# Kernel optimization log

Hardware: AMD Instinct MI355X
Metric: run time of the kernel (lower is better)

Reference implementation:

```python
import jax, jax.numpy as jnp
import numpy as np

H = 8
HID = 512
DH = HID // H
EPS = 1e-5


def _ln(x, g, b):
    mu = jnp.mean(x, axis=-1, keepdims=True)
    var = jnp.mean(jnp.square(x - mu), axis=-1, keepdims=True)
    return (x - mu) * jax.lax.rsqrt(var + EPS) * g + b


def setup_inputs() -> dict:
    key = jax.random.key(0)
    ks = jax.random.split(key, 40)
    L, M, P, D = 4096, 1024, 4096, 512

    def xav(k, shp):
        lim = np.sqrt(6.0 / (shp[0] + shp[1]))
        return jax.random.uniform(k, shp, jnp.float32, -lim, lim)

    inp = {
        'lncRNA_embedding': jax.random.normal(ks[0], (L, D), jnp.float32),
        'miRNA_embedding': jax.random.normal(ks[1], (M, D), jnp.float32),
        'protein_embedding': jax.random.normal(ks[2], (P, D), jnp.float32),
        'lncRNA_miRNA_matrix': jax.random.randint(ks[3], (L, M), 0, 2, jnp.int32),
        'protein_miRNA_matrix': jax.random.randint(ks[4], (P, M), 0, 2, jnp.int32),
    }
    names = ['Wl', 'Wm', 'Wp', 'Wql', 'Wkl', 'Wvl', 'Wqp', 'Wkp', 'Wvp']
    for i, n in enumerate(names):
        inp[n] = xav(ks[5 + i], (HID, HID))
        inp['b' + n[1:]] = jnp.zeros((HID,), jnp.float32)
    inp['Wml'] = xav(ks[20], (2 * HID, D // 2))
    inp['bml'] = jnp.zeros((D // 2,), jnp.float32)
    inp['Wmp'] = xav(ks[21], (2 * HID, D // 2))
    inp['bmp'] = jnp.zeros((D // 2,), jnp.float32)
    inp['g1'] = jnp.ones((D // 2,), jnp.float32)
    inp['be1'] = jnp.zeros((D // 2,), jnp.float32)
    inp['g2'] = jnp.ones((D // 2,), jnp.float32)
    inp['be2'] = jnp.zeros((D // 2,), jnp.float32)
    # first three linears take dim-D input (D == HID here)
    return inp


def reference(lncRNA_embedding, miRNA_embedding, protein_embedding,
              lncRNA_miRNA_matrix, protein_miRNA_matrix,
              Wl, bl, Wm, bm, Wp, bp,
              Wql, bql, Wkl, bkl, Wvl, bvl,
              Wqp, bqp, Wkp, bkp, Wvp, bvp,
              Wml, bml, Wmp, bmp, g1, be1, g2, be2):
    L = lncRNA_embedding.shape[0]
    M = miRNA_embedding.shape[0]
    P = protein_embedding.shape[0]

    lt = lncRNA_embedding @ Wl + bl          # [L, HID]
    mt = miRNA_embedding @ Wm + bm           # [M, HID]
    pt = protein_embedding @ Wp + bp         # [P, HID]

    def heads(x, W, b, n):
        return (x @ W + b).reshape(n, H, DH)

    Ql = heads(lt, Wql, bql, L)              # [L, H, DH]
    Kl = heads(mt, Wkl, bkl, M)
    Vl = heads(mt, Wvl, bvl, M)
    Qp = heads(pt, Wqp, bqp, P)
    Kp = heads(mt, Wkp, bkp, M)
    Vp = heads(mt, Wvp, bvp, M)

    scale = 1.0 / np.sqrt(DH)
    sl = jnp.einsum('lhd,mhd->hlm', Ql, Kl) * scale      # [H, L, M]
    sl = jnp.where(lncRNA_miRNA_matrix[None] == 0, -1e9, sl)
    awl = jax.nn.softmax(sl, axis=-1)

    sp = jnp.einsum('phd,mhd->hpm', Qp, Kp) * scale      # [H, P, M]
    sp = jnp.where(protein_miRNA_matrix[None] == 0, -1e9, sp)
    awp = jax.nn.softmax(sp, axis=-1)

    ctx_l = jax.nn.relu(jnp.einsum('hlm,mhd->lhd', awl, Vl).reshape(L, HID))
    ctx_p = jax.nn.relu(jnp.einsum('hpm,mhd->phd', awp, Vp).reshape(P, HID))

    mutual = jnp.einsum('hlm,hpm->lp', awl, awp) / H     # [L, P]

    fin_l = ctx_l + mutual @ ctx_p
    fin_p = ctx_p + mutual.T @ ctx_l

    out_l = _ln(jnp.concatenate([lt, fin_l], axis=-1) @ Wml + bml, g1, be1)
    out_p = _ln(jnp.concatenate([fin_p, pt], axis=-1) @ Wmp + bmp, g2, be2)
    return out_l, out_p
```

## Files before the change

### kernel.cpp

```cpp
#include <hip/hip_runtime.h>
#include <hip/hip_bf16.h>

using bf16 = __hip_bfloat16;
typedef __attribute__((ext_vector_type(8))) short short8;
typedef __attribute__((ext_vector_type(4))) float floatx4;
typedef __attribute__((ext_vector_type(8))) unsigned short ushort8;
typedef __attribute__((ext_vector_type(4))) int i32x4;
typedef __attribute__((ext_vector_type(8))) int i32x8;

__device__ __forceinline__ float b2f(unsigned short u) {
    union { unsigned int i; float f; } x; x.i = ((unsigned int)u) << 16; return x.f;
}

__device__ __forceinline__ void async16(const void* g, void* l) {
    __builtin_amdgcn_global_load_lds((const __attribute__((address_space(1))) void*)g,
                                     (__attribute__((address_space(3))) void*)l,
                                     16, 0, 0);
}

__device__ __forceinline__ unsigned char f2e4m3(float f) {
    unsigned s = (__float_as_uint(f) >> 24) & 0x80u;
    f = fminf(fabsf(f), 448.f);
    if (f < 0.015625f) {
        int d = (int)rintf(f * 512.f);
        return (unsigned char)(s | (unsigned)d);
    }
    int E = (int)((__float_as_uint(f) >> 23) & 255u) - 127;
    float ulp_inv = __uint_as_float((unsigned)(127 + 3 - E) << 23);
    int m = (int)rintf(f * ulp_inv);
    int n = (m == 16) ? ((E + 8) << 3) : (((E + 7) << 3) + (m - 8));
    if (n > 0x7E) n = 0x7E;
    return (unsigned char)(s | (unsigned)n);
}

__device__ __forceinline__ bool sniff_wave(const unsigned short* p) {
    const int lane = threadIdx.x & 63;
    int wild = 0;
#pragma unroll
    for (int j = 0; j < 4; ++j) {
        float a = fabsf(b2f(p[lane * 4 + j]));
        wild += !(a <= 1e4f);
    }
#pragma unroll
    for (int o = 1; o < 64; o <<= 1) wild += __shfl_xor(wild, o);
    return wild > 16;
}

struct Cvt { const void* src; bf16* dst; int n; };
struct PrepArgs {
    Cvt cv[18];
    const void* tsrc[11];
    bf16* tdst[11];
    const unsigned short* sn;
};

__global__ __launch_bounds__(256) void prep(PrepArgs a) {
    const bool f32 = sniff_wave(a.sn);
    const int y = blockIdx.y;
    __shared__ bf16 tile[32][33];

    if (y < 18) {
        const Cvt c = a.cv[y];
        const int stride = gridDim.x * 256 * 8;
        for (int i = (blockIdx.x * 256 + threadIdx.x) * 8; i < c.n; i += stride) {
            if (f32) {
                const float* s = (const float*)c.src + i;
#pragma unroll
                for (int j = 0; j < 8; ++j) c.dst[i + j] = __float2bfloat16(s[j]);
            } else {
                *(ushort8*)((unsigned short*)c.dst + i) =
                    *(const ushort8*)((const unsigned short*)c.src + i);
            }
        }
        return;
    }

    const int tx = threadIdx.x & 31;
    const int ty = threadIdx.x >> 5;
    if (y < 27) {
        const void* in = a.tsrc[y - 18];
        bf16* out = a.tdst[y - 18];
        const int bc = (blockIdx.x & 15) * 32;
        const int br = (blockIdx.x >> 4) * 32;
#pragma unroll
        for (int i = 0; i < 32; i += 8) {
            const size_t idx = (size_t)(br + ty + i) * 512 + bc + tx;
            tile[ty + i][tx] = f32 ? __float2bfloat16(((const float*)in)[idx])
                                   : ((const bf16*)in)[idx];
        }
        __syncthreads();
#pragma unroll
        for (int i = 0; i < 32; i += 8)
            out[(size_t)(bc + ty + i) * 512 + br + tx] = tile[tx][ty + i];
    } else {
        const void* in = a.tsrc[y - 27 + 9];
        bf16* out = a.tdst[y - 27 + 9];
        const int bc = (blockIdx.x & 7) * 32;
        const int br = (blockIdx.x >> 3) * 32;
#pragma unroll
        for (int i = 0; i < 32; i += 8) {
            const size_t idx = (size_t)(br + ty + i) * 256 + bc + tx;
            tile[ty + i][tx] = f32 ? __float2bfloat16(((const float*)in)[idx])
                                   : ((const bf16*)in)[idx];
        }
        __syncthreads();
#pragma unroll
        for (int i = 0; i < 32; i += 8)
            out[(size_t)(bc + ty + i) * 1024 + br + tx] = tile[tx][ty + i];
    }
}

struct SegTab { const bf16* W[3]; const bf16* bias[3]; bf16* C[3]; int ldc[3]; int rs[3]; };

__global__ __launch_bounds__(256) void gemm_bt_seg(
    const bf16* __restrict__ A, SegTab T, int K)
{
    constexpr int TM = 2, TN = 2;
    __align__(16) __shared__ bf16 As[64 * 64];
    __align__(16) __shared__ bf16 Bs[64 * 64];

    const int lane = threadIdx.x & 63;
    const int wv   = threadIdx.x >> 6;
    const int gm   = blockIdx.y * 64;
    const int seg  = (gm >= 5120) ? 2 : ((gm >= 4096) ? 1 : 0);
    const bf16* B  = T.W[seg];
    const bf16* bias = T.bias[seg];
    bf16* C        = T.C[seg];
    const int ldc  = T.ldc[seg];
    const int m_base = gm - T.rs[seg];
    const int n_base = blockIdx.x * 64;
    const int wm0 = (wv >> 1) * 32;
    const int wn0 = (wv & 1) * 32;

    floatx4 zero = {0.f, 0.f, 0.f, 0.f};
    floatx4 acc[TM][TN];
#pragma unroll
    for (int mt = 0; mt < TM; ++mt)
#pragma unroll
        for (int nt = 0; nt < TN; ++nt) acc[mt][nt] = zero;

    const int sr  = lane >> 3;
    const int sce = ((lane & 7) ^ sr) * 8;
    const int fr  = lane & 15;
    const int q   = lane >> 4;
    const int sw  = fr & 7;

    for (int k0 = 0; k0 < K; k0 += 64) {
#pragma unroll
        for (int cc = 0; cc < 2; ++cc) {
            const int r0t = (wv + cc * 4) * 8;
            async16(A + (size_t)(gm + r0t + sr) * 512 + k0 + sce, &As[r0t * 64]);
            async16(B + (size_t)(n_base + r0t + sr) * 512 + k0 + sce, &Bs[r0t * 64]);
        }
        __syncthreads();
#pragma unroll
        for (int s = 0; s < 2; ++s) {
            const int off = ((s * 4 + q) ^ sw) * 8;
            short8 af[TM], bfr[TN];
#pragma unroll
            for (int mt = 0; mt < TM; ++mt)
                af[mt] = *(const short8*)&As[(wm0 + mt * 16 + fr) * 64 + off];
#pragma unroll
            for (int nt = 0; nt < TN; ++nt)
                bfr[nt] = *(const short8*)&Bs[(wn0 + nt * 16 + fr) * 64 + off];
#pragma unroll
            for (int mt = 0; mt < TM; ++mt)
#pragma unroll
                for (int nt = 0; nt < TN; ++nt)
                    acc[mt][nt] = __builtin_amdgcn_mfma_f32_16x16x32_bf16(
                        af[mt], bfr[nt], acc[mt][nt], 0, 0, 0);
        }
        __syncthreads();
    }

    const int er = lane >> 4;
    const int ec = lane & 15;
#pragma unroll
    for (int nt = 0; nt < TN; ++nt) {
        const int col = n_base + wn0 + nt * 16 + ec;
        const float bv = __bfloat162float(bias[col]);
#pragma unroll
        for (int mt = 0; mt < TM; ++mt)
#pragma unroll
            for (int r = 0; r < 4; ++r) {
                const int row = m_base + wm0 + mt * 16 + er * 4 + r;
                C[(size_t)row * ldc + col] = __float2bfloat16(acc[mt][nt][r] + bv);
            }
    }
}

struct BtArgs { const bf16* A; const bf16* B; void* C; const bf16* bias;
                int lda, ldb, ldc; };
struct BtSet { BtArgs s[3]; };

template <bool F32OUT, bool REMAP2>
__global__ __launch_bounds__(256) void gemm_btx(BtSet P, int K, float scale)
{
    constexpr int TM = 2, TN = 2;
    __align__(16) __shared__ bf16 As[64 * 64];
    __align__(16) __shared__ bf16 Bs[64 * 64];

    const BtArgs g = P.s[blockIdx.z];
    int bx = blockIdx.x, by = blockIdx.y;
    if (REMAP2 && blockIdx.z == 2) {
        const int flat = by * gridDim.x + bx;
        bx = flat & 31; by = flat >> 5;
    }
    const int lane = threadIdx.x & 63;
    const int wv   = threadIdx.x >> 6;
    const int m_base = by * 64;
    const int n_base = bx * 64;
    const int wm0 = (wv >> 1) * 32;
    const int wn0 = (wv & 1) * 32;

    floatx4 zero = {0.f, 0.f, 0.f, 0.f};
    floatx4 acc[TM][TN];
#pragma unroll
    for (int mt = 0; mt < TM; ++mt)
#pragma unroll
        for (int nt = 0; nt < TN; ++nt) acc[mt][nt] = zero;

    const int sr  = lane >> 3;
    const int sce = ((lane & 7) ^ sr) * 8;
    const int fr  = lane & 15;
    const int q   = lane >> 4;
    const int sw  = fr & 7;

    for (int k0 = 0; k0 < K; k0 += 64) {
#pragma unroll
        for (int cc = 0; cc < 2; ++cc) {
            const int r0t = (wv + cc * 4) * 8;
            async16(g.A + (size_t)(m_base + r0t + sr) * g.lda + k0 + sce, &As[r0t * 64]);
            async16(g.B + (size_t)(n_base + r0t + sr) * g.ldb + k0 + sce, &Bs[r0t * 64]);
        }
        __syncthreads();
#pragma unroll
        for (int s = 0; s < 2; ++s) {
            const int off = ((s * 4 + q) ^ sw) * 8;
            short8 af[TM], bfr[TN];
#pragma unroll
            for (int mt = 0; mt < TM; ++mt)
                af[mt] = *(const short8*)&As[(wm0 + mt * 16 + fr) * 64 + off];
#pragma unroll
            for (int nt = 0; nt < TN; ++nt)
                bfr[nt] = *(const short8*)&Bs[(wn0 + nt * 16 + fr) * 64 + off];
#pragma unroll
            for (int mt = 0; mt < TM; ++mt)
#pragma unroll
                for (int nt = 0; nt < TN; ++nt)
                    acc[mt][nt] = __builtin_amdgcn_mfma_f32_16x16x32_bf16(
                        af[mt], bfr[nt], acc[mt][nt], 0, 0, 0);
        }
        __syncthreads();
    }

    const int er = lane >> 4;
    const int ec = lane & 15;
#pragma unroll
    for (int nt = 0; nt < TN; ++nt) {
        const int col = n_base + wn0 + nt * 16 + ec;
        const float bv = __bfloat162float(g.bias[col]);
#pragma unroll
        for (int mt = 0; mt < TM; ++mt)
#pragma unroll
            for (int r = 0; r < 4; ++r) {
                const int row = m_base + wm0 + mt * 16 + er * 4 + r;
                const float v = acc[mt][nt][r] * scale + bv;
                if constexpr (F32OUT)
                    ((float*)g.C)[(size_t)row * g.ldc + col] = v;
                else
                    ((bf16*)g.C)[(size_t)row * g.ldc + col] = __float2bfloat16(v);
            }
    }
}

struct ScArgs { const bf16* Q; const bf16* K; const int* mask; unsigned char* aw;
                unsigned char* awt; };
struct ScSet { ScArgs s[2]; const bf16* vsrc[2]; unsigned char* vdst[2]; };

__global__ __launch_bounds__(256) void scores_v8(ScSet P, int ldk, float scale)
{
    __shared__ float wred[16][4];
    __shared__ float wsum[16][4];
    __shared__ float tile[32][33];

    const int flat = blockIdx.x;
    if (flat >= 4096) {
        const int f2   = flat - 4096;
        const int side = f2 >> 9;
        const int rem  = f2 & 511;
        const bf16* in = P.vsrc[side];
        unsigned char* out = P.vdst[side];
        const int bc = (rem & 15) * 32;
        const int br = (rem >> 4) * 32;
        const int tx = threadIdx.x & 31;
        const int ty = threadIdx.x >> 5;
#pragma unroll
        for (int i = 0; i < 32; i += 8)
            tile[ty + i][tx] =
                __bfloat162float(in[(size_t)(br + ty + i) * 2048 + bc + tx]) * 4.0f;
        __syncthreads();
#pragma unroll
        for (int i = 0; i < 32; i += 8)
            out[(size_t)(bc + ty + i) * 1024 + br + tx] = f2e4m3(tile[tx][ty + i]);
        return;
    }

    const int s    = (flat >> 3) & 3;
    const int unit = (flat >> 5) * 8 + (flat & 7);
    const int side = unit >> 9;
    const int h    = (unit >> 6) & 7;
    const int r0   = (unit & 63) * 64 + s * 16;

    const ScArgs g = P.s[side];
    const int t    = threadIdx.x;
    const int lane = t & 63;
    const int w    = t >> 6;
    const int fr   = lane & 15;
    const int fq   = lane >> 4;
    const int cbase = w * 256;

    const short* Qs = (const short*)g.Q + (size_t)(r0 + fr) * 512 + h * 64 + fq * 8;
    short8 a0 = *(const short8*)(Qs);
    short8 a1 = *(const short8*)(Qs + 32);

    floatx4 accs[16];
    const short* Kb = (const short*)g.K + h * 64 + fq * 8;
#pragma unroll
    for (int c = 0; c < 16; ++c) {
        const int krow = cbase + c * 16 + fr;
        short8 b0 = *(const short8*)(Kb + (size_t)krow * ldk);
        short8 b1 = *(const short8*)(Kb + (size_t)krow * ldk + 32);
        floatx4 acc = {0.f, 0.f, 0.f, 0.f};
        acc = __builtin_amdgcn_mfma_f32_16x16x32_bf16(a0, b0, acc, 0, 0, 0);
        acc = __builtin_amdgcn_mfma_f32_16x16x32_bf16(a1, b1, acc, 0, 0, 0);
        accs[c] = acc;
    }

    float mxr[4] = {-3e38f, -3e38f, -3e38f, -3e38f};
#pragma unroll
    for (int c = 0; c < 16; ++c) {
        const int col = cbase + c * 16 + fr;
#pragma unroll
        for (int r = 0; r < 4; ++r) {
            const int row = r0 + fq * 4 + r;
            float v = (g.mask[(size_t)row * 1024 + col] == 0) ? -1e9f
                                                              : accs[c][r] * scale;
            accs[c][r] = v;
            mxr[r] = fmaxf(mxr[r], v);
        }
    }
#pragma unroll
    for (int o = 1; o < 16; o <<= 1)
#pragma unroll
        for (int r = 0; r < 4; ++r) mxr[r] = fmaxf(mxr[r], __shfl_xor(mxr[r], o));
    if (fr == 0)
#pragma unroll
        for (int r = 0; r < 4; ++r) wred[fq * 4 + r][w] = mxr[r];
    __syncthreads();

    float mx[4], sm[4] = {0.f, 0.f, 0.f, 0.f};
#pragma unroll
    for (int r = 0; r < 4; ++r) {
        const int row = fq * 4 + r;
        mx[r] = fmaxf(fmaxf(wred[row][0], wred[row][1]),
                      fmaxf(wred[row][2], wred[row][3]));
    }
#pragma unroll
    for (int c = 0; c < 16; ++c)
#pragma unroll
        for (int r = 0; r < 4; ++r) {
            float e = __expf(accs[c][r] - mx[r]);
            accs[c][r] = e;
            sm[r] += e;
        }
#pragma unroll
    for (int o = 1; o < 16; o <<= 1)
#pragma unroll
        for (int r = 0; r < 4; ++r) sm[r] += __shfl_xor(sm[r], o);
    if (fr == 0)
#pragma unroll
        for (int r = 0; r < 4; ++r) wsum[fq * 4 + r][w] = sm[r];
    __syncthreads();

    float inv[4];
#pragma unroll
    for (int r = 0; r < 4; ++r) {
        const int row = fq * 4 + r;
        inv[r] = 32.0f / (wsum[row][0] + wsum[row][1] + wsum[row][2] + wsum[row][3]);
    }
#pragma unroll
    for (int c = 0; c < 16; ++c) {
        const int col = cbase + c * 16 + fr;
        unsigned int pk = 0;
#pragma unroll
        for (int r = 0; r < 4; ++r) {
            const int row = r0 + fq * 4 + r;
            const unsigned char qv = f2e4m3(accs[c][r] * inv[r]);
            g.aw[(size_t)row * 8192 + h * 1024 + col] = qv;
            pk |= (unsigned)qv << (8 * r);
        }
        *(unsigned int*)(g.awt + (size_t)(h * 1024 + col) * 4096 + r0 + fq * 4) = pk;
    }
}

struct B8Args { const unsigned char* A; const unsigned char* B; bf16* C;
                unsigned char* CT; };
struct B8Pair { B8Args s[2]; };

__global__ __launch_bounds__(256) void gemm_bt8_ctx(
    B8Pair P, int lda, long long a_kshift, int ldb, int ldc, int ldct,
    int K, float scale)
{
    constexpr int TM = 2, TN = 2;
    __align__(16) __shared__ unsigned char As[64 * 64];
    __align__(16) __shared__ unsigned char Bs[64 * 64];

    const B8Args g = P.s[blockIdx.z];
    const int lane = threadIdx.x & 63;
    const int wv   = threadIdx.x >> 6;
    const int m_base = blockIdx.y * 64;
    const int n_base = blockIdx.x * 64;
    const unsigned char* A = g.A + (long long)blockIdx.x * a_kshift;

    const int wm0 = (wv >> 1) * 32;
    const int wn0 = (wv & 1) * 32;

    floatx4 zero = {0.f, 0.f, 0.f, 0.f};
    floatx4 acc[TM][TN];
#pragma unroll
    for (int mt = 0; mt < TM; ++mt)
#pragma unroll
        for (int nt = 0; nt < TN; ++nt) acc[mt][nt] = zero;

    const int ar = lane >> 2;
    const int ac = (((lane & 3) ^ (ar & 3)) * 16);
    const int fr = lane & 15;
    const int q  = lane >> 4;
    const int sw = fr & 3;

    for (int k0 = 0; k0 < K; k0 += 64) {
        async16(A + (size_t)(m_base + wv * 16 + ar) * lda + k0 + ac, &As[wv * 16 * 64]);
        async16(g.B + (size_t)(n_base + wv * 16 + ar) * ldb + k0 + ac, &Bs[wv * 16 * 64]);
        __syncthreads();
#pragma unroll
        for (int s = 0; s < 2; ++s) {
            const int boff = (((s * 2 + (q >> 1)) ^ sw) * 16) + (q & 1) * 8;
            long af[TM], bfr[TN];
#pragma unroll
            for (int mt = 0; mt < TM; ++mt)
                af[mt] = *(const long*)&As[(wm0 + mt * 16 + fr) * 64 + boff];
#pragma unroll
            for (int nt = 0; nt < TN; ++nt)
                bfr[nt] = *(const long*)&Bs[(wn0 + nt * 16 + fr) * 64 + boff];
#pragma unroll
            for (int mt = 0; mt < TM; ++mt)
#pragma unroll
                for (int nt = 0; nt < TN; ++nt)
                    acc[mt][nt] = __builtin_amdgcn_mfma_f32_16x16x32_fp8_fp8(
                        af[mt], bfr[nt], acc[mt][nt], 0, 0, 0);
        }
        __syncthreads();
    }

    const int er = lane >> 4;
    const int ec = lane & 15;
#pragma unroll
    for (int nt = 0; nt < TN; ++nt) {
        const int col = n_base + wn0 + nt * 16 + ec;
#pragma unroll
        for (int mt = 0; mt < TM; ++mt) {
            const int rowb = m_base + wm0 + mt * 16 + er * 4;
            unsigned int pk = 0;
#pragma unroll
            for (int r = 0; r < 4; ++r) {
                float v = fmaxf(acc[mt][nt][r] * scale, 0.f);
                g.C[(size_t)(rowb + r) * ldc + col] = __float2bfloat16(v);
                pk |= (unsigned)f2e4m3(v * 16.0f) << (8 * r);
            }
            *(unsigned int*)(g.CT + (size_t)col * ldct + rowb) = pk;
        }
    }
}

struct MxArgs { const unsigned char* A; const unsigned char* B; void* C;
                const bf16* Cz; unsigned char* CT; };
struct MxPair { MxArgs s[2]; };

template <int BM, int BN, bool ADDC0, bool FP8OUT, bool TOUT>
__global__ __launch_bounds__(256, 2) void gemm_bt8mx(
    MxPair P, int lda, int ldb, int ldc, int ldc0, int ldct, int K, float scale)
{
    constexpr int WM = BM / 2;
    constexpr int WN = BN / 2;
    constexpr int TM = WM / 16;
    constexpr int TN = WN / 16;

    __align__(16) __shared__ unsigned char As[BM * 128];
    __align__(16) __shared__ unsigned char Bs[BN * 128];

    const MxArgs g = P.s[blockIdx.z];
    const int lane = threadIdx.x & 63;
    const int wv   = threadIdx.x >> 6;
    const int m_base = blockIdx.y * BM;
    const int n_base = blockIdx.x * BN;

    const int wm0 = (wv >> 1) * WM;
    const int wn0 = (wv & 1) * WN;

    floatx4 zero = {0.f, 0.f, 0.f, 0.f};
    floatx4 acc[TM][TN];
#pragma unroll
    for (int mt = 0; mt < TM; ++mt)
#pragma unroll
        for (int nt = 0; nt < TN; ++nt) acc[mt][nt] = zero;

    const int sr = lane >> 3;
    const int sc = ((lane & 7) ^ sr) * 16;
    const int fr = lane & 15;
    const int q  = lane >> 4;
    const int sw = fr & 7;

    for (int k0 = 0; k0 < K; k0 += 128) {
#pragma unroll
        for (int cc = 0; cc < BM / 32; ++cc) {
            const int r0t = (wv + cc * 4) * 8;
            async16(g.A + (size_t)(m_base + r0t + sr) * lda + k0 + sc, &As[r0t * 128]);
        }
#pragma unroll
        for (int cc = 0; cc < BN / 32; ++cc) {
            const int r0t = (wv + cc * 4) * 8;
            async16(g.B + (size_t)(n_base + r0t + sr) * ldb + k0 + sc, &Bs[r0t * 128]);
        }
        __syncthreads();

        i32x8 af[TM];
#pragma unroll
        for (int mt = 0; mt < TM; ++mt) {
            const unsigned char* rp = &As[(wm0 + mt * 16 + fr) * 128];
            i32x4 lo = *(const i32x4*)(rp + (((q * 2 + 0) ^ sw) * 16));
            i32x4 hi = *(const i32x4*)(rp + (((q * 2 + 1) ^ sw) * 16));
            af[mt] = __builtin_shufflevector(lo, hi, 0, 1, 2, 3, 4, 5, 6, 7);
        }
#pragma unroll
        for (int nt = 0; nt < TN; ++nt) {
            const unsigned char* rp = &Bs[(wn0 + nt * 16 + fr) * 128];
            i32x4 lo = *(const i32x4*)(rp + (((q * 2 + 0) ^ sw) * 16));
            i32x4 hi = *(const i32x4*)(rp + (((q * 2 + 1) ^ sw) * 16));
            i32x8 bf8 = __builtin_shufflevector(lo, hi, 0, 1, 2, 3, 4, 5, 6, 7);
#pragma unroll
            for (int mt = 0; mt < TM; ++mt)
                acc[mt][nt] = __builtin_amdgcn_mfma_scale_f32_16x16x128_f8f6f4(
                    af[mt], bf8, acc[mt][nt], 0, 0, 0, 127, 0, 127);
        }
        __syncthreads();
    }

    const int er = lane >> 4;
    const int ec = lane & 15;
#pragma unroll
    for (int nt = 0; nt < TN; ++nt) {
        const int col = n_base + wn0 + nt * 16 + ec;
#pragma unroll
        for (int mt = 0; mt < TM; ++mt) {
            const int rowb = m_base + wm0 + mt * 16 + er * 4;
            unsigned int pk = 0;
#pragma unroll
            for (int r = 0; r < 4; ++r) {
                float v = acc[mt][nt][r] * scale;
                if constexpr (ADDC0)
                    v += __bfloat162float(g.Cz[(size_t)(rowb + r) * ldc0 + col]);
                if constexpr (FP8OUT) {
                    const unsigned char qv = f2e4m3(v);
                    ((unsigned char*)g.C)[(size_t)(rowb + r) * ldc + col] = qv;
                    if constexpr (TOUT) pk |= (unsigned)qv << (8 * r);
                } else {
                    ((bf16*)g.C)[(size_t)(rowb + r) * ldc + col] = __float2bfloat16(v);
                }
            }
            if constexpr (TOUT)
                *(unsigned int*)(g.CT + (size_t)col * ldct + rowb) = pk;
        }
    }
}

__global__ __launch_bounds__(256) void ln_all(
    const float* __restrict__ X,
    const bf16* __restrict__ g1, const bf16* __restrict__ be1,
    const bf16* __restrict__ g2, const bf16* __restrict__ be2,
    void* __restrict__ out, const unsigned short* __restrict__ sn)
{
    const bool f32 = sniff_wave(sn);
    const int lane = threadIdx.x & 63;
    const int wv   = threadIdx.x >> 6;
    const int row  = blockIdx.x * 4 + wv;
    const bf16* gg = (row >= 4096) ? g2 : g1;
    const bf16* bb = (row >= 4096) ? be2 : be1;
    const float* x = X + (size_t)row * 256;
    float v[4], s = 0.f, s2 = 0.f;
#pragma unroll
    for (int i = 0; i < 4; ++i) {
        v[i] = x[lane + 64 * i];
        s += v[i]; s2 += v[i] * v[i];
    }
#pragma unroll
    for (int o = 1; o < 64; o <<= 1) { s += __shfl_xor(s, o); s2 += __shfl_xor(s2, o); }
    const float mu  = s * (1.0f / 256.0f);
    const float var = fmaxf(s2 * (1.0f / 256.0f) - mu * mu, 0.0f);
    const float inv = rsqrtf(var + 1e-5f);
#pragma unroll
    for (int i = 0; i < 4; ++i) {
        const int c = lane + 64 * i;
        const float y = (v[i] - mu) * inv * __bfloat162float(gg[c]) + __bfloat162float(bb[c]);
        if (f32) ((float*)out)[(size_t)row * 256 + c] = y;
        else     ((bf16*)out)[(size_t)row * 256 + c] = __float2bfloat16(y);
    }
}

extern "C" void kernel_launch(void* const* d_in, const int* in_sizes, int n_in,
                              void* d_out, int out_size, void* d_ws, size_t ws_size,
                              hipStream_t stream)
{
    const int L = 4096, Mm = 1024, P = 4096;

    const int* mask_l = (const int*)d_in[3];
    const int* mask_p = (const int*)d_in[4];
    const unsigned short* sn = (const unsigned short*)d_in[0];

    char* ws = (char*)d_ws;
    size_t off = 0;
    auto alloc = [&](size_t bytes) {
        void* p = ws + off; off += (bytes + 255) & ~(size_t)255; return p;
    };

    bf16* wt_all = (bf16*)alloc((size_t)9 * 512 * 512 * 2);
    bf16* WmlT   = (bf16*)alloc(1024 * 256 * 2);
    bf16* WmpT   = (bf16*)alloc(1024 * 256 * 2);
    bf16* b_l    = (bf16*)alloc(512 * 2);
    bf16* b_m    = (bf16*)alloc(512 * 2);
    bf16* b_p    = (bf16*)alloc(512 * 2);
    bf16* b_ql   = (bf16*)alloc(512 * 2);
    bf16* b_qp   = (bf16*)alloc(512 * 2);
    bf16* bcat   = (bf16*)alloc(2048 * 2);
    bf16* bml_c  = (bf16*)alloc(256 * 2);
    bf16* bmp_c  = (bf16*)alloc(256 * 2);
    bf16* g1c    = (bf16*)alloc(256 * 2);
    bf16* be1c   = (bf16*)alloc(256 * 2);
    bf16* g2c    = (bf16*)alloc(256 * 2);
    bf16* be2c   = (bf16*)alloc(256 * 2);
    bf16* emb_all = (bf16*)alloc((size_t)(L + Mm + P) * 512 * 2);
    bf16* embl   = emb_all;
    bf16* embm   = emb_all + (size_t)L * 512;
    bf16* embp   = embm + (size_t)Mm * 512;
    bf16* cat_l  = (bf16*)alloc((size_t)L * 1024 * 2);
    bf16* cat_p  = (bf16*)alloc((size_t)P * 1024 * 2);
    bf16* mt     = (bf16*)alloc((size_t)Mm * 512 * 2);
    bf16* Ql     = (bf16*)alloc((size_t)L * 512 * 2);
    bf16* Qp     = (bf16*)alloc((size_t)P * 512 * 2);
    bf16* kvcat  = (bf16*)alloc((size_t)Mm * 2048 * 2);
    unsigned char* V8lT = (unsigned char*)alloc((size_t)512 * Mm);
    unsigned char* V8pT = (unsigned char*)alloc((size_t)512 * Mm);
    bf16* ctx_l  = (bf16*)alloc((size_t)L * 512 * 2);
    bf16* ctx_p  = (bf16*)alloc((size_t)P * 512 * 2);
    unsigned char* ctx8lT = (unsigned char*)alloc((size_t)512 * L);
    unsigned char* ctx8pT = (unsigned char*)alloc((size_t)512 * P);
    unsigned char* awlT8  = (unsigned char*)alloc((size_t)8192 * 4096);
    unsigned char* awpT8  = (unsigned char*)alloc((size_t)8192 * 4096);
    unsigned char* awl8 = (unsigned char*)alloc((size_t)L * 8192);
    unsigned char* awp8 = (unsigned char*)alloc((size_t)P * 8192);
    unsigned char* T1lT = (unsigned char*)emb_all;
    unsigned char* T1pT = (unsigned char*)emb_all + (size_t)512 * 8192;
    float* tmp1 = (float*)awp8;

    PrepArgs pa;
    pa.sn = sn;
    pa.cv[0]  = { d_in[0],  embl, L * 512 };
    pa.cv[1]  = { d_in[1],  embm, Mm * 512 };
    pa.cv[2]  = { d_in[2],  embp, P * 512 };
    pa.cv[3]  = { d_in[6],  b_l,  512 };
    pa.cv[4]  = { d_in[8],  b_m,  512 };
    pa.cv[5]  = { d_in[10], b_p,  512 };
    pa.cv[6]  = { d_in[12], b_ql, 512 };
    pa.cv[7]  = { d_in[18], b_qp, 512 };
    pa.cv[8]  = { d_in[14], bcat,        512 };
    pa.cv[9]  = { d_in[16], bcat + 512,  512 };
    pa.cv[10] = { d_in[20], bcat + 1024, 512 };
    pa.cv[11] = { d_in[22], bcat + 1536, 512 };
    pa.cv[12] = { d_in[24], bml_c, 256 };
    pa.cv[13] = { d_in[26], bmp_c, 256 };
    pa.cv[14] = { d_in[27], g1c,  256 };
    pa.cv[15] = { d_in[28], be1c, 256 };
    pa.cv[16] = { d_in[29], g2c,  256 };
    pa.cv[17] = { d_in[30], be2c, 256 };
    const int slot_of[9] = {0, 1, 2, 3, 5, 6, 4, 7, 8};
    for (int i = 0; i < 9; ++i) {
        pa.tsrc[i] = d_in[5 + 2 * i];
        pa.tdst[i] = wt_all + (size_t)slot_of[i] * 512 * 512;
    }
    pa.tsrc[9]  = d_in[23]; pa.tdst[9]  = WmlT;
    pa.tsrc[10] = d_in[25]; pa.tdst[10] = WmpT;
    prep<<<dim3(256, 29), 256, 0, stream>>>(pa);

    bf16* WlT  = wt_all;
    bf16* WmT  = wt_all + (size_t)1 * 512 * 512;
    bf16* WpT  = wt_all + (size_t)2 * 512 * 512;
    bf16* WqlT = wt_all + (size_t)3 * 512 * 512;
    bf16* WqpT = wt_all + (size_t)4 * 512 * 512;
    bf16* WkvT = wt_all + (size_t)5 * 512 * 512;

    SegTab st;
    st.W[0] = WlT;  st.bias[0] = b_l; st.C[0] = cat_l;       st.ldc[0] = 1024; st.rs[0] = 0;
    st.W[1] = WmT;  st.bias[1] = b_m; st.C[1] = mt;          st.ldc[1] = 512;  st.rs[1] = 4096;
    st.W[2] = WpT;  st.bias[2] = b_p; st.C[2] = cat_p + 512; st.ldc[2] = 1024; st.rs[2] = 5120;
    gemm_bt_seg<<<dim3(8, 144), 256, 0, stream>>>(emb_all, st, 512);

    BtSet qs;
    qs.s[0] = { cat_l,       WqlT, Ql,    b_ql, 1024, 512, 512 };
    qs.s[1] = { cat_p + 512, WqpT, Qp,    b_qp, 1024, 512, 512 };
    qs.s[2] = { mt,          WkvT, kvcat, bcat, 512,  512, 2048 };
    gemm_btx<false, true><<<dim3(8, 64, 3), 256, 0, stream>>>(qs, 512, 1.0f);

    ScSet sc;
    sc.s[0] = { Ql, kvcat,        mask_l, awl8, awlT8 };
    sc.s[1] = { Qp, kvcat + 1024, mask_p, awp8, awpT8 };
    sc.vsrc[0] = kvcat + 512;  sc.vdst[0] = V8lT;
    sc.vsrc[1] = kvcat + 1536; sc.vdst[1] = V8pT;
    scores_v8<<<dim3(5120), 256, 0, stream>>>(sc, 2048, 0.125f);

    B8Pair cx = { { { awl8, V8lT, ctx_l, ctx8lT },
                    { awp8, V8pT, ctx_p, ctx8pT } } };
    gemm_bt8_ctx<<<dim3(8, 64, 2), 256, 0, stream>>>(
        cx, 8192, 1024, 1024, 512, 4096, 1024, 1.0f / 128.0f);

    MxPair t1 = { { { ctx8pT, awpT8, T1lT, nullptr, nullptr },
                    { ctx8lT, awlT8, T1pT, nullptr, nullptr } } };
    gemm_bt8mx<128, 256, false, true, false><<<dim3(32, 4, 2), 256, 0, stream>>>(
        t1, 4096, 4096, 8192, 0, 0, 4096, 1.0f / 128.0f);

    MxPair fn = { { { awl8, T1lT, cat_l + 512, ctx_l, nullptr },
                    { awp8, T1pT, cat_p,       ctx_p, nullptr } } };
    gemm_bt8mx<128, 128, true, false, false><<<dim3(4, 32, 2), 256, 0, stream>>>(
        fn, 8192, 8192, 1024, 512, 0, 8192, 1.0f / 1024.0f);

    BtSet fp;
    fp.s[0] = { cat_l, WmlT, tmp1,                   bml_c, 1024, 1024, 256 };
    fp.s[1] = { cat_p, WmpT, tmp1 + (size_t)L * 256, bmp_c, 1024, 1024, 256 };
    fp.s[2] = fp.s[0];
    gemm_btx<true, false><<<dim3(4, 64, 2), 256, 0, stream>>>(fp, 1024, 1.0f);

    ln_all<<<dim3(2048), 256, 0, stream>>>(tmp1, g1c, be1c, g2c, be2c, d_out, sn);
}
```

Measured before the change: 508.5 us.

## Use hardware packed FP8 conversion and blocked layout for transposed attention weights

Replaces the software float-to-e4m3 routine with the packed hardware conversion builtin wherever four values are quantised together. The transposed attention-weight buffer is stored in 16-row blocks, so each scores block writes one contiguous 16-byte chunk per column instead of strided 4-byte pieces. The mx GEMM gains a k-block stride parameter so it can read that blocked layout, and the scores grid mapping is simplified to match. This aims to cut ALU work in the epilogues and make the awT writes coalesced. The risk is that the hardware conversion rounds or saturates differently from the custom routine.

```diff
diff --git a/kernel.cpp b/kernel.cpp
--- a/kernel.cpp
+++ b/kernel.cpp
@@ -31,6 +31,17 @@
     int n = (m == 16) ? ((E + 8) << 3) : (((E + 7) << 3) + (m - 8));
     if (n > 0x7E) n = 0x7E;
     return (unsigned char)(s | (unsigned)n);
+}
+
+__device__ __forceinline__ unsigned int pk4_e4m3(float a, float b, float c, float d) {
+#if __has_builtin(__builtin_amdgcn_cvt_pk_fp8_f32)
+    int p = __builtin_amdgcn_cvt_pk_fp8_f32(a, b, 0, false);
+    p = __builtin_amdgcn_cvt_pk_fp8_f32(c, d, p, true);
+    return (unsigned int)p;
+#else
+    return (unsigned)f2e4m3(a) | ((unsigned)f2e4m3(b) << 8) |
+           ((unsigned)f2e4m3(c) << 16) | ((unsigned)f2e4m3(d) << 24);
+#endif
 }
 
 __device__ __forceinline__ bool sniff_wave(const unsigned short* p) {
@@ -300,17 +311,19 @@
             tile[ty + i][tx] =
                 __bfloat162float(in[(size_t)(br + ty + i) * 2048 + bc + tx]) * 4.0f;
         __syncthreads();
-#pragma unroll
-        for (int i = 0; i < 32; i += 8)
-            out[(size_t)(bc + ty + i) * 1024 + br + tx] = f2e4m3(tile[tx][ty + i]);
+        const unsigned int vp = pk4_e4m3(tile[tx][ty], tile[tx][ty + 8],
+                                         tile[tx][ty + 16], tile[tx][ty + 24]);
+#pragma unroll
+        for (int i = 0; i < 4; ++i)
+            out[(size_t)(bc + ty + i * 8) * 1024 + br + tx] =
+                (unsigned char)(vp >> (8 * i));
         return;
     }
 
-    const int s    = (flat >> 3) & 3;
-    const int unit = (flat >> 5) * 8 + (flat & 7);
-    const int side = unit >> 9;
-    const int h    = (unit >> 6) & 7;
-    const int r0   = (unit & 63) * 64 + s * 16;
+    const int side = flat >> 11;
+    const int idx  = flat & 2047;
+    const int h    = idx >> 8;
+    const int r0   = (idx & 255) * 16;
 
     const ScArgs g = P.s[side];
     const int t    = threadIdx.x;
@@ -389,18 +402,17 @@
         const int row = fq * 4 + r;
         inv[r] = 32.0f / (wsum[row][0] + wsum[row][1] + wsum[row][2] + wsum[row][3]);
     }
+    unsigned char* awtb = g.awt + (size_t)(r0 >> 4) * 131072 + fq * 4;
 #pragma unroll
     for (int c = 0; c < 16; ++c) {
         const int col = cbase + c * 16 + fr;
-        unsigned int pk = 0;
-#pragma unroll
-        for (int r = 0; r < 4; ++r) {
-            const int row = r0 + fq * 4 + r;
-            const unsigned char qv = f2e4m3(accs[c][r] * inv[r]);
-            g.aw[(size_t)row * 8192 + h * 1024 + col] = qv;
-            pk |= (unsigned)qv << (8 * r);
-        }
-        *(unsigned int*)(g.awt + (size_t)(h * 1024 + col) * 4096 + r0 + fq * 4) = pk;
+        const unsigned int pk = pk4_e4m3(accs[c][0] * inv[0], accs[c][1] * inv[1],
+                                         accs[c][2] * inv[2], accs[c][3] * inv[3]);
+#pragma unroll
+        for (int r = 0; r < 4; ++r)
+            g.aw[(size_t)(r0 + fq * 4 + r) * 8192 + h * 1024 + col] =
+                (unsigned char)(pk >> (8 * r));
+        *(unsigned int*)(awtb + (size_t)(h * 1024 + col) * 16) = pk;
     }
 }
 
@@ -471,13 +483,15 @@
 #pragma unroll
         for (int mt = 0; mt < TM; ++mt) {
             const int rowb = m_base + wm0 + mt * 16 + er * 4;
-            unsigned int pk = 0;
-#pragma unroll
-            for (int r = 0; r < 4; ++r) {
-                float v = fmaxf(acc[mt][nt][r] * scale, 0.f);
-                g.C[(size_t)(rowb + r) * ldc + col] = __float2bfloat16(v);
-                pk |= (unsigned)f2e4m3(v * 16.0f) << (8 * r);
-            }
+            float v0 = fmaxf(acc[mt][nt][0] * scale, 0.f);
+            float v1 = fmaxf(acc[mt][nt][1] * scale, 0.f);
+            float v2 = fmaxf(acc[mt][nt][2] * scale, 0.f);
+            float v3 = fmaxf(acc[mt][nt][3] * scale, 0.f);
+            g.C[(size_t)(rowb + 0) * ldc + col] = __float2bfloat16(v0);
+            g.C[(size_t)(rowb + 1) * ldc + col] = __float2bfloat16(v1);
+            g.C[(size_t)(rowb + 2) * ldc + col] = __float2bfloat16(v2);
+            g.C[(size_t)(rowb + 3) * ldc + col] = __float2bfloat16(v3);
+            const unsigned int pk = pk4_e4m3(v0 * 16.f, v1 * 16.f, v2 * 16.f, v3 * 16.f);
             *(unsigned int*)(g.CT + (size_t)col * ldct + rowb) = pk;
         }
     }
@@ -489,7 +503,8 @@
 
 template <int BM, int BN, bool ADDC0, bool FP8OUT, bool TOUT>
 __global__ __launch_bounds__(256, 2) void gemm_bt8mx(
-    MxPair P, int lda, int ldb, int ldc, int ldc0, int ldct, int K, float scale)
+    MxPair P, int lda, int ldb, int ldbk, int ldc, int ldc0, int ldct,
+    int K, float scale)
 {
     constexpr int WM = BM / 2;
     constexpr int WN = BN / 2;
@@ -530,7 +545,8 @@
 #pragma unroll
         for (int cc = 0; cc < BN / 32; ++cc) {
             const int r0t = (wv + cc * 4) * 8;
-            async16(g.B + (size_t)(n_base + r0t + sr) * ldb + k0 + sc, &Bs[r0t * 128]);
+            async16(g.B + (size_t)(n_base + r0t + sr) * ldb +
+                        (size_t)((k0 + sc) >> 4) * ldbk, &Bs[r0t * 128]);
         }
         __syncthreads();
 
@@ -564,22 +580,26 @@
 #pragma unroll
         for (int mt = 0; mt < TM; ++mt) {
             const int rowb = m_base + wm0 + mt * 16 + er * 4;
-            unsigned int pk = 0;
+            float v[4];
 #pragma unroll
             for (int r = 0; r < 4; ++r) {
-                float v = acc[mt][nt][r] * scale;
+                v[r] = acc[mt][nt][r] * scale;
                 if constexpr (ADDC0)
-                    v += __bfloat162float(g.Cz[(size_t)(rowb + r) * ldc0 + col]);
-                if constexpr (FP8OUT) {
-                    const unsigned char qv = f2e4m3(v);
-                    ((unsigned char*)g.C)[(size_t)(rowb + r) * ldc + col] = qv;
-                    if constexpr (TOUT) pk |= (unsigned)qv << (8 * r);
-                } else {
-                    ((bf16*)g.C)[(size_t)(rowb + r) * ldc + col] = __float2bfloat16(v);
-                }
+                    v[r] += __bfloat162float(g.Cz[(size_t)(rowb + r) * ldc0 + col]);
             }
-            if constexpr (TOUT)
-                *(unsigned int*)(g.CT + (size_t)col * ldct + rowb) = pk;
+            if constexpr (FP8OUT) {
+                const unsigned int pk = pk4_e4m3(v[0], v[1], v[2], v[3]);
+#pragma unroll
+                for (int r = 0; r < 4; ++r)
+                    ((unsigned char*)g.C)[(size_t)(rowb + r) * ldc + col] =
+                        (unsigned char)(pk >> (8 * r));
+                if constexpr (TOUT)
+                    *(unsigned int*)(g.CT + (size_t)col * ldct + rowb) = pk;
+            } else {
+#pragma unroll
+                for (int r = 0; r < 4; ++r)
+                    ((bf16*)g.C)[(size_t)(rowb + r) * ldc + col] = __float2bfloat16(v[r]);
+            }
         }
     }
 }
@@ -735,12 +755,12 @@
     MxPair t1 = { { { ctx8pT, awpT8, T1lT, nullptr, nullptr },
                     { ctx8lT, awlT8, T1pT, nullptr, nullptr } } };
     gemm_bt8mx<128, 256, false, true, false><<<dim3(32, 4, 2), 256, 0, stream>>>(
-        t1, 4096, 4096, 8192, 0, 0, 4096, 1.0f / 128.0f);
+        t1, 4096, 16, 131072, 8192, 0, 0, 4096, 1.0f / 128.0f);
 
     MxPair fn = { { { awl8, T1lT, cat_l + 512, ctx_l, nullptr },
                     { awp8, T1pT, cat_p,       ctx_p, nullptr } } };
     gemm_bt8mx<128, 128, true, false, false><<<dim3(4, 32, 2), 256, 0, stream>>>(
-        fn, 8192, 8192, 1024, 512, 0, 8192, 1.0f / 1024.0f);
+        fn, 8192, 8192, 16, 1024, 512, 0, 8192, 1.0f / 1024.0f);
 
     BtSet fp;
     fp.s[0] = { cat_l, WmlT, tmp1,                   bml_c, 1024, 1024, 256 };
```

New measurement: 477.8 us. 6.0% less time.
